# Performance work log

Measured on AMD Instinct MI355X. Metric: run time of the kernel, lower is better.

The kernel has to match this reference:

```python
import jax, jax.numpy as jnp
import numpy as np

N_USER, N_ITEM, D, K, E = 80000, 40000, 128, 10, 2000000

def _mlp(x, w1, b1, w2, b2, w3, b3):
    # MLP from source: linear->tanh->linear->tanh->linear->L2 normalize (eval mode, dropout off)
    x = jnp.tanh(x @ w1 + b1)
    x = jnp.tanh(x @ w2 + b2)
    x = x @ w3 + b3
    return x / jnp.maximum(jnp.linalg.norm(x, axis=-1, keepdims=True), 1e-12)

def setup_inputs() -> dict:
    key = jax.random.key(0)
    ks = jax.random.split(key, 24)
    s = 0.05
    inp = {
        'uemb_s': jax.random.normal(ks[0], (N_USER, D), jnp.float32),
        'iemb_s': jax.random.normal(ks[1], (N_ITEM, D), jnp.float32),
        'uemb_t': jax.random.normal(ks[2], (N_USER, D), jnp.float32),
        'u_emb_sp': jax.random.normal(ks[3], (N_USER, D), jnp.float32),
        'edge_user': jax.random.randint(ks[4], (E,), 0, N_USER, jnp.int32),
        'edge_item': jax.random.randint(ks[5], (E,), 0, N_ITEM, jnp.int32),
        # meta nets
        'Wu': jax.random.normal(ks[6], (4 * D, D), jnp.float32) * s,
        'bu': jnp.zeros((D,), jnp.float32),
        'Wi': jax.random.normal(ks[7], (2 * D, D), jnp.float32) * s,
        'bi': jnp.zeros((D,), jnp.float32),
        # mlp1: D -> D*K -> D//2 -> D*K
        'm1w1': jax.random.normal(ks[8], (D, D * K), jnp.float32) * s,
        'm1b1': jnp.zeros((D * K,), jnp.float32),
        'm1w2': jax.random.normal(ks[9], (D * K, D // 2), jnp.float32) * s,
        'm1b2': jnp.zeros((D // 2,), jnp.float32),
        'm1w3': jax.random.normal(ks[10], (D // 2, D * K), jnp.float32) * s,
        'm1b3': jnp.zeros((D * K,), jnp.float32),
        # mlp2: D -> D*K -> D//2 -> D*K
        'm2w1': jax.random.normal(ks[11], (D, D * K), jnp.float32) * s,
        'm2b1': jnp.zeros((D * K,), jnp.float32),
        'm2w2': jax.random.normal(ks[12], (D * K, D // 2), jnp.float32) * s,
        'm2b2': jnp.zeros((D // 2,), jnp.float32),
        'm2w3': jax.random.normal(ks[13], (D // 2, D * K), jnp.float32) * s,
        'm2b3': jnp.zeros((D * K,), jnp.float32),
    }
    return inp

def reference(uemb_s, iemb_s, uemb_t, u_emb_sp, edge_user, edge_item,
              Wu, bu, Wi, bi,
              m1w1, m1b1, m1w2, m1b2, m1w3, m1b3,
              m2w1, m2b1, m2w2, m2b2, m2w3, m2b3):
    # spmm with all-ones values == gather + segment_sum over the bipartite edge list
    neighbors_u = jax.ops.segment_sum(iemb_s[edge_item], edge_user, num_segments=N_USER)  # [U, D]
    tmp_embu = jax.lax.stop_gradient(
        jnp.concatenate([uemb_s, uemb_t, u_emb_sp, neighbors_u], axis=1)) @ Wu + bu       # [U, D]
    neighbors_i = jax.ops.segment_sum(((uemb_s + u_emb_sp) * 0.5)[edge_user], edge_item,
                                      num_segments=N_ITEM)                               # [I, D]
    tmp_embi = jax.lax.stop_gradient(
        jnp.concatenate([iemb_s, neighbors_i], axis=1)) @ Wi + bi                         # [I, D]
    metau = _mlp(tmp_embu, m1w1, m1b1, m1w2, m1b2, m1w3, m1b3).reshape(-1, D, K)          # [U, D, K]
    metai = _mlp(tmp_embi, m2w1, m2b1, m2w2, m2b2, m2w3, m2b3).reshape(-1, K, D)          # [I, K, D]
    meta_biasu = jnp.mean(metau, axis=0)  # [D, K]
    meta_biasi = jnp.mean(metai, axis=0)  # [K, D]
    low_weightu = jax.nn.softmax(metau + meta_biasu, axis=1)
    low_weighti = jax.nn.softmax(metai + meta_biasi, axis=1)
    return (low_weightu, low_weighti)
```

## Files before the change

kernel.cpp:

```cpp
#include <hip/hip_runtime.h>
#include <hip/hip_bf16.h>

#define D_ 128
#define DK_ 1280
#define K_ 10

typedef __attribute__((ext_vector_type(8))) short bh8;
typedef __attribute__((ext_vector_type(4))) short bh4;
typedef __attribute__((ext_vector_type(4))) float f32x4;

__device__ __forceinline__ short f2b(float f) {
    unsigned u = __builtin_bit_cast(unsigned, f);
    u += 0x7fffu + ((u >> 16) & 1u);
    return (short)(u >> 16);
}
__device__ __forceinline__ float b2f(short s) {
    unsigned u = ((unsigned)(unsigned short)s) << 16;
    return __builtin_bit_cast(float, u);
}
__device__ __forceinline__ float tanh_fast(float x) {
    float e = __expf(2.f * x);
    return 1.f - __fdividef(2.f, e + 1.f);
}
__device__ __forceinline__ f32x4 mfma16(bh8 a, bh8 b, f32x4 c) {
    return __builtin_amdgcn_mfma_f32_16x16x32_bf16(a, b, c, 0, 0, 0);
}

__device__ __forceinline__ int blk_excl_scan(int v, int t) {
    __shared__ int wp[4];
    int lane = t & 63, w = t >> 6;
    int s = v;
    for (int o = 1; o < 64; o <<= 1) {
        int pv = __shfl_up(s, o);
        if (lane >= o) s += pv;
    }
    if (lane == 63) wp[w] = s;
    __syncthreads();
    if (t == 0) {
        int a = 0;
#pragma unroll
        for (int k = 0; k < 4; ++k) { int x = wp[k]; wp[k] = a; a += x; }
    }
    __syncthreads();
    int r = s - v + wp[w];
    __syncthreads();
    return r;
}

__global__ __launch_bounds__(256) void cvt_all(
    const float* __restrict__ us, const float* __restrict__ ut,
    const float* __restrict__ usp, const float* __restrict__ is_,
    short* __restrict__ usb, short* __restrict__ utb,
    short* __restrict__ uspb, short* __restrict__ uavg, short* __restrict__ isb,
    int n4u, int n4i)
{
    int i = blockIdx.x * 256 + threadIdx.x;
    if (i < n4u) {
        float4 a = ((const float4*)us)[i];
        float4 b = ((const float4*)ut)[i];
        float4 c = ((const float4*)usp)[i];
        bh4 sa, sb, sc, sv;
        sa[0] = f2b(a.x); sa[1] = f2b(a.y); sa[2] = f2b(a.z); sa[3] = f2b(a.w);
        sb[0] = f2b(b.x); sb[1] = f2b(b.y); sb[2] = f2b(b.z); sb[3] = f2b(b.w);
        sc[0] = f2b(c.x); sc[1] = f2b(c.y); sc[2] = f2b(c.z); sc[3] = f2b(c.w);
        sv[0] = f2b(0.5f * (a.x + c.x)); sv[1] = f2b(0.5f * (a.y + c.y));
        sv[2] = f2b(0.5f * (a.z + c.z)); sv[3] = f2b(0.5f * (a.w + c.w));
        ((bh4*)usb)[i] = sa; ((bh4*)utb)[i] = sb;
        ((bh4*)uspb)[i] = sc; ((bh4*)uavg)[i] = sv;
    } else if (i < n4u + n4i) {
        int j = i - n4u;
        float4 v = ((const float4*)is_)[j];
        bh4 s;
        s[0] = f2b(v.x); s[1] = f2b(v.y); s[2] = f2b(v.z); s[3] = f2b(v.w);
        ((bh4*)isb)[j] = s;
    }
}

struct PackArgs {
    const float* W[8];
    short* o[8];
    int K[8];
    int N[8];
};
__global__ __launch_bounds__(256) void pack_all(PackArgs pa)
{
    int seg = blockIdx.y;
    int K = pa.K[seg], N = pa.N[seg];
    int total = K * N;
    int o = blockIdx.x * 256 + threadIdx.x;
    if (o >= total) return;
    const float* W = pa.W[seg];
    short* out = pa.o[seg];
    int j    = o & 7;
    int lane = (o >> 3) & 63;
    int rest = o >> 9;
    int KK = K >> 5;
    int kk = rest % KK;
    int tile = rest / KK;
    int k = kk * 32 + (lane >> 4) * 8 + j;
    int n = tile * 16 + (lane & 15);
    out[o] = f2b(W[(size_t)k * N + n]);
}

__global__ __launch_bounds__(256) void bhist_kernel(
    const int* __restrict__ eu, const int* __restrict__ ei,
    int* __restrict__ bcu, int* __restrict__ bci,
    int E, int shu, int shi, int nbu, int nbi)
{
    __shared__ int hu[160], hi[160];
    int t = threadIdx.x;
    int base = blockIdx.x * 4096;
    if (t < 160) { hu[t] = 0; hi[t] = 0; }
    __syncthreads();
    int n = min(4096, E - base);
#pragma unroll 4
    for (int k = 0; k < 16; ++k) {
        int idx = k * 256 + t;
        if (idx < n) {
            atomicAdd(&hu[eu[base + idx] >> shu], 1);
            atomicAdd(&hi[ei[base + idx] >> shi], 1);
        }
    }
    __syncthreads();
    if (t < nbu && hu[t]) atomicAdd(&bcu[t], hu[t]);
    if (t < nbi && hi[t]) atomicAdd(&bci[t], hi[t]);
}

__global__ __launch_bounds__(256) void binit_kernel(
    const int* __restrict__ bcu, int* __restrict__ gcu, int* __restrict__ bbu, int nbu,
    const int* __restrict__ bci, int* __restrict__ gci, int* __restrict__ bbi, int nbi,
    int E)
{
    int t = threadIdx.x;
    {
        int v = (t < nbu) ? bcu[t] : 0;
        int ex = blk_excl_scan(v, t);
        if (t < nbu) { gcu[t] = ex; bbu[t] = ex; }
        if (t == 0) bbu[nbu] = E;
    }
    __syncthreads();
    {
        int v = (t < nbi) ? bci[t] : 0;
        int ex = blk_excl_scan(v, t);
        if (t < nbi) { gci[t] = ex; bbi[t] = ex; }
        if (t == 0) bbi[nbi] = E;
    }
}

__global__ __launch_bounds__(256) void partition_kernel(
    const int* __restrict__ eu, const int* __restrict__ ei,
    int* __restrict__ gcu, int* __restrict__ gci,
    uint2* __restrict__ ebu, uint2* __restrict__ ebi,
    int E, int shu, int shi, int nbu, int nbi)
{
    __shared__ int hu[160], hi[160];
    int t = threadIdx.x;
    int base = blockIdx.x * 4096;
    if (t < 160) { hu[t] = 0; hi[t] = 0; }
    __syncthreads();
    int n = min(4096, E - base);
    int us[16], is_[16];
#pragma unroll 4
    for (int k = 0; k < 16; ++k) {
        int idx = k * 256 + t;
        if (idx < n) {
            us[k] = eu[base + idx];
            is_[k] = ei[base + idx];
            atomicAdd(&hu[us[k] >> shu], 1);
            atomicAdd(&hi[is_[k] >> shi], 1);
        } else us[k] = -1;
    }
    __syncthreads();
    if (t < nbu) { int c = hu[t]; hu[t] = c ? atomicAdd(&gcu[t], c) : 0; }
    if (t < nbi) { int c = hi[t]; hi[t] = c ? atomicAdd(&gci[t], c) : 0; }
    __syncthreads();
#pragma unroll 4
    for (int k = 0; k < 16; ++k) {
        if (us[k] >= 0) {
            int p1 = atomicAdd(&hu[us[k] >> shu], 1);
            ebu[p1] = make_uint2((unsigned)us[k], (unsigned)is_[k]);
            int p2 = atomicAdd(&hi[is_[k] >> shi], 1);
            ebi[p2] = make_uint2((unsigned)is_[k], (unsigned)us[k]);
        }
    }
}

__global__ __launch_bounds__(256) void fill2_all(
    const uint2* __restrict__ ebu, const int* __restrict__ bbu,
    int* __restrict__ off_u, int* __restrict__ end_u, int* __restrict__ adj_u,
    int NBU, int U,
    const uint2* __restrict__ ebi, const int* __restrict__ bbi,
    int* __restrict__ off_i, int* __restrict__ end_i, int* __restrict__ adj_i, int I)
{
    __shared__ int lcnt[512];
    __shared__ int lcur[512];
    bool isU = (int)blockIdx.x < NBU;
    const uint2* ebuf = isU ? ebu : ebi;
    const int* bbase  = isU ? bbu : bbi;
    int* off  = isU ? off_u : off_i;
    int* end_ = isU ? end_u : end_i;
    int* adj  = isU ? adj_u : adj_i;
    int span_sh = isU ? 9 : 8;
    int nrows = isU ? U : I;
    int b = isU ? blockIdx.x : blockIdx.x - NBU;

    int t = threadIdx.x;
    int rbase = b << span_sh;
    int span = min(1 << span_sh, nrows - rbase);
    int regbeg = bbase[b], regend = bbase[b + 1];
    for (int j = t; j < span; j += 256) lcnt[j] = 0;
    __syncthreads();
    for (int e = regbeg + t; e < regend; e += 256)
        atomicAdd(&lcnt[ebuf[e].x - rbase], 1);
    __syncthreads();
    int c0 = (2 * t < span) ? lcnt[2 * t] : 0;
    int c1 = (2 * t + 1 < span) ? lcnt[2 * t + 1] : 0;
    int ex = blk_excl_scan(c0 + c1, t);
    if (2 * t < span) {
        int beg = regbeg + ex;
        off[rbase + 2 * t] = beg;
        end_[rbase + 2 * t] = beg + c0;
        lcur[2 * t] = beg;
    }
    if (2 * t + 1 < span) {
        int beg = regbeg + ex + c0;
        off[rbase + 2 * t + 1] = beg;
        end_[rbase + 2 * t + 1] = beg + c1;
        lcur[2 * t + 1] = beg;
    }
    __syncthreads();
    for (int e = regbeg + t; e < regend; e += 256) {
        uint2 p = ebuf[e];
        int slot = atomicAdd(&lcur[p.x - rbase], 1);
        adj[slot] = (int)p.y;
    }
}

__global__ __launch_bounds__(256) void gather_all(
    const short* __restrict__ embU, const short* __restrict__ embI,
    const int* __restrict__ off_u, const int* __restrict__ end_u, const int* __restrict__ adj_u,
    const int* __restrict__ off_i, const int* __restrict__ end_i, const int* __restrict__ adj_i,
    short* __restrict__ nub, short* __restrict__ nib, int U, int I)
{
    int gw = (blockIdx.x * 256 + threadIdx.x) >> 6;
    int lane = threadIdx.x & 63;
    const short* emb; const int *offp, *endp, *adjp; short* outp; int row;
    if (gw < U)          { emb = embU; offp = off_u; endp = end_u; adjp = adj_u; outp = nub; row = gw; }
    else if (gw < U + I) { emb = embI; offp = off_i; endp = end_i; adjp = adj_i; outp = nib; row = gw - U; }
    else return;

    int beg = offp[row], end = endp[row];
    float ax = 0.f, ay = 0.f;
    int j = beg;
    for (; j + 3 < end; j += 4) {
        unsigned a = *(const unsigned*)(emb + (size_t)adjp[j]     * D_ + lane * 2);
        unsigned b = *(const unsigned*)(emb + (size_t)adjp[j + 1] * D_ + lane * 2);
        unsigned c = *(const unsigned*)(emb + (size_t)adjp[j + 2] * D_ + lane * 2);
        unsigned d = *(const unsigned*)(emb + (size_t)adjp[j + 3] * D_ + lane * 2);
        ax += b2f((short)(a & 0xffff)) + b2f((short)(b & 0xffff))
            + b2f((short)(c & 0xffff)) + b2f((short)(d & 0xffff));
        ay += b2f((short)(a >> 16)) + b2f((short)(b >> 16))
            + b2f((short)(c >> 16)) + b2f((short)(d >> 16));
    }
    for (; j < end; ++j) {
        unsigned a = *(const unsigned*)(emb + (size_t)adjp[j] * D_ + lane * 2);
        ax += b2f((short)(a & 0xffff));
        ay += b2f((short)(a >> 16));
    }
    unsigned o = ((unsigned)(unsigned short)f2b(ay) << 16) | (unsigned short)(unsigned)f2b(ax);
    *(unsigned*)(outp + (size_t)row * D_ + lane * 2) = o;
}

struct MlpArgs {
    const short *uA0, *uA1, *uA2, *uA3;
    const short *iA0, *iA1;
    const short *uWg, *uW1, *uW2, *uW3;
    const short *iWg, *iW1, *iW2, *iW3;
    const float *ubg, *ub1, *ub2, *ub3;
    const float *ibg, *ib1, *ib2, *ib3;
    short *uY, *iY;
    float *uNrm, *iNrm;
    int UB;
};

__global__ __launch_bounds__(256, 4) void fused_mlp_all(MlpArgs P)
{
    __shared__ char pool[35328];
    short* x2   = (short*)pool;
    short* h1q  = (short*)(pool + 8704);
    short* h2   = (short*)(pool + 29696);
    float* wred = (float*)(pool + 34304);

    const int t = threadIdx.x;
    const int l = t & 63;
    const int w = t >> 6;
    const int lr = l & 15;
    const int lg = l >> 4;

    const bool isU = (int)blockIdx.x < P.UB;
    const int bid = isU ? (int)blockIdx.x : (int)blockIdx.x - P.UB;
    const size_t rb0 = (size_t)bid * 32;
    const int KKG  = isU ? 16 : 8;
    const short* Wg = isU ? P.uWg : P.iWg;
    const short* W1 = isU ? P.uW1 : P.iW1;
    const short* W2 = isU ? P.uW2 : P.iW2;
    const short* W3 = isU ? P.uW3 : P.iW3;
    const float* bg = isU ? P.ubg : P.ibg;
    const float* b1 = isU ? P.ub1 : P.ib1;
    const float* b2 = isU ? P.ub2 : P.ib2;
    const float* b3 = isU ? P.ub3 : P.ib3;
    short* Ybf = isU ? P.uY : P.iY;
    float* Nrm = isU ? P.uNrm : P.iNrm;
    const short* srcs[4];
    if (isU) { srcs[0] = P.uA0; srcs[1] = P.uA1; srcs[2] = P.uA2; srcs[3] = P.uA3; }
    else     { srcs[0] = P.iA0; srcs[1] = P.iA1; srcs[2] = P.iA0; srcs[3] = P.iA1; }

    {
        f32x4 acc[2][2] = {{{0,0,0,0},{0,0,0,0}},{{0,0,0,0},{0,0,0,0}}};
        const short* wp = Wg + (size_t)(2 * w) * KKG * 512 + l * 8;
        const short* wq = wp + (size_t)KKG * 512;
        for (int kk = 0; kk < KKG; ++kk) {
            const short* src = srcs[kk >> 2];
            int coff = (kk & 3) * 32 + lg * 8;
            bh8 x0 = *(const bh8*)(src + (rb0 + lr) * D_ + coff);
            bh8 x1 = *(const bh8*)(src + (rb0 + 16 + lr) * D_ + coff);
            bh8 w0 = *(const bh8*)wp; wp += 512;
            bh8 w1 = *(const bh8*)wq; wq += 512;
            acc[0][0] = mfma16(w0, x0, acc[0][0]);
            acc[1][0] = mfma16(w0, x1, acc[1][0]);
            acc[0][1] = mfma16(w1, x0, acc[0][1]);
            acc[1][1] = mfma16(w1, x1, acc[1][1]);
        }
        float4 c0 = *(const float4*)(bg + (2 * w) * 16 + lg * 4);
        float4 c1 = *(const float4*)(bg + (2 * w + 1) * 16 + lg * 4);
#pragma unroll
        for (int rg = 0; rg < 2; ++rg) {
            bh4 p0, p1;
            p0[0] = f2b(acc[rg][0][0] + c0.x); p0[1] = f2b(acc[rg][0][1] + c0.y);
            p0[2] = f2b(acc[rg][0][2] + c0.z); p0[3] = f2b(acc[rg][0][3] + c0.w);
            p1[0] = f2b(acc[rg][1][0] + c1.x); p1[1] = f2b(acc[rg][1][1] + c1.y);
            p1[2] = f2b(acc[rg][1][2] + c1.z); p1[3] = f2b(acc[rg][1][3] + c1.w);
            *(bh4*)(x2 + (rg * 16 + lr) * 136 + (2 * w) * 16 + lg * 4) = p0;
            *(bh4*)(x2 + (rg * 16 + lr) * 136 + (2 * w + 1) * 16 + lg * 4) = p1;
        }
    }
    __syncthreads();

    bh8 xf[2][4];
#pragma unroll
    for (int rg = 0; rg < 2; ++rg)
#pragma unroll
        for (int kk = 0; kk < 4; ++kk)
            xf[rg][kk] = *(const bh8*)(x2 + (rg * 16 + lr) * 136 + kk * 32 + lg * 8);

    f32x4 c2[2][2] = {{{0,0,0,0},{0,0,0,0}},{{0,0,0,0},{0,0,0,0}}};
#pragma unroll 1
    for (int q = 0; q < 4; ++q) {
        const short* wp = W1 + (size_t)(q * 20 + w * 5) * 2048 + l * 8;
        const float* bp = b1 + (q * 20 + w * 5) * 16 + lg * 4;
#pragma unroll 1
        for (int tt = 0; tt < 5; ++tt) {
            f32x4 a0 = {0,0,0,0}, a1 = a0;
#pragma unroll
            for (int kk = 0; kk < 4; ++kk) {
                bh8 wf = *(const bh8*)wp; wp += 512;
                a0 = mfma16(wf, xf[0][kk], a0);
                a1 = mfma16(wf, xf[1][kk], a1);
            }
            float4 bv = *(const float4*)bp; bp += 16;
            bh4 pk0, pk1;
            pk0[0] = f2b(tanh_fast(a0[0] + bv.x)); pk0[1] = f2b(tanh_fast(a0[1] + bv.y));
            pk0[2] = f2b(tanh_fast(a0[2] + bv.z)); pk0[3] = f2b(tanh_fast(a0[3] + bv.w));
            pk1[0] = f2b(tanh_fast(a1[0] + bv.x)); pk1[1] = f2b(tanh_fast(a1[1] + bv.y));
            pk1[2] = f2b(tanh_fast(a1[2] + bv.z)); pk1[3] = f2b(tanh_fast(a1[3] + bv.w));
            int lt = w * 5 + tt;
            *(bh4*)(h1q + lr * 328 + lt * 16 + lg * 4) = pk0;
            *(bh4*)(h1q + (16 + lr) * 328 + lt * 16 + lg * 4) = pk1;
        }
        __syncthreads();
        const short* wp2 = W2 + (size_t)(w * 40 + q * 10) * 512 + l * 8;
        const short* hq0 = h1q + lr * 328 + lg * 8;
        const short* hq1 = h1q + (16 + lr) * 328 + lg * 8;
#pragma unroll 2
        for (int kk = 0; kk < 10; ++kk) {
            bh8 wf = *(const bh8*)wp2; wp2 += 512;
            bh8 h0 = *(const bh8*)(hq0 + kk * 32);
            bh8 h1v = *(const bh8*)(hq1 + kk * 32);
            if (kk & 1) { c2[0][1] = mfma16(wf, h0, c2[0][1]); c2[1][1] = mfma16(wf, h1v, c2[1][1]); }
            else        { c2[0][0] = mfma16(wf, h0, c2[0][0]); c2[1][0] = mfma16(wf, h1v, c2[1][0]); }
        }
        __syncthreads();
    }

    {
        float4 bv = *(const float4*)(b2 + w * 16 + lg * 4);
#pragma unroll
        for (int rg = 0; rg < 2; ++rg) {
            bh4 p2;
            p2[0] = f2b(tanh_fast(c2[rg][0][0] + c2[rg][1][0] + bv.x));
            p2[1] = f2b(tanh_fast(c2[rg][0][1] + c2[rg][1][1] + bv.y));
            p2[2] = f2b(tanh_fast(c2[rg][0][2] + c2[rg][1][2] + bv.z));
            p2[3] = f2b(tanh_fast(c2[rg][0][3] + c2[rg][1][3] + bv.w));
            *(bh4*)(h2 + (rg * 16 + lr) * 72 + w * 16 + lg * 4) = p2;
        }
    }
    __syncthreads();

    {
        bh8 hf[2][2];
#pragma unroll
        for (int rg = 0; rg < 2; ++rg) {
            hf[rg][0] = *(const bh8*)(h2 + (rg * 16 + lr) * 72 + lg * 8);
            hf[rg][1] = *(const bh8*)(h2 + (rg * 16 + lr) * 72 + 32 + lg * 8);
        }
        float ssq0 = 0.f, ssq1 = 0.f;
        const short* wp3 = W3 + (size_t)(w * 20) * 1024 + l * 8;
        const float* bp3 = b3 + w * 320 + lg * 4;
        short* dst0 = Ybf + (rb0 + lr) * DK_ + w * 320 + lg * 4;
        short* dst1 = Ybf + (rb0 + 16 + lr) * DK_ + w * 320 + lg * 4;
#pragma unroll 2
        for (int tt = 0; tt < 20; ++tt) {
            bh8 w0 = *(const bh8*)(wp3 + tt * 1024);
            bh8 w1 = *(const bh8*)(wp3 + tt * 1024 + 512);
            float4 bv = *(const float4*)(bp3 + tt * 16);
            f32x4 a0 = {0,0,0,0}, a1 = a0;
            a0 = mfma16(w0, hf[0][0], a0); a0 = mfma16(w1, hf[0][1], a0);
            a1 = mfma16(w0, hf[1][0], a1); a1 = mfma16(w1, hf[1][1], a1);
            float v00 = a0[0] + bv.x, v01 = a0[1] + bv.y, v02 = a0[2] + bv.z, v03 = a0[3] + bv.w;
            float v10 = a1[0] + bv.x, v11 = a1[1] + bv.y, v12 = a1[2] + bv.z, v13 = a1[3] + bv.w;
            ssq0 = fmaf(v00, v00, ssq0); ssq0 = fmaf(v01, v01, ssq0);
            ssq0 = fmaf(v02, v02, ssq0); ssq0 = fmaf(v03, v03, ssq0);
            ssq1 = fmaf(v10, v10, ssq1); ssq1 = fmaf(v11, v11, ssq1);
            ssq1 = fmaf(v12, v12, ssq1); ssq1 = fmaf(v13, v13, ssq1);
            bh4 o0, o1;
            o0[0] = f2b(v00); o0[1] = f2b(v01); o0[2] = f2b(v02); o0[3] = f2b(v03);
            o1[0] = f2b(v10); o1[1] = f2b(v11); o1[2] = f2b(v12); o1[3] = f2b(v13);
            *(bh4*)(dst0 + tt * 16) = o0;
            *(bh4*)(dst1 + tt * 16) = o1;
        }
        ssq0 += __shfl_xor(ssq0, 16); ssq0 += __shfl_xor(ssq0, 32);
        ssq1 += __shfl_xor(ssq1, 16); ssq1 += __shfl_xor(ssq1, 32);
        if (l < 16) {
            wred[w * 32 + l] = ssq0;
            wred[w * 32 + 16 + l] = ssq1;
        }
    }
    __syncthreads();
    if (t < 32) {
        float s = wred[t] + wred[32 + t] + wred[64 + t] + wred[96 + t];
        Nrm[rb0 + t] = 1.f / fmaxf(sqrtf(s), 1e-12f);
    }
}

__global__ __launch_bounds__(256) void finalize_bias(
    const short* __restrict__ Yu, const short* __restrict__ Yi,
    const float* __restrict__ nrmU, const float* __restrict__ nrmI,
    float* __restrict__ bsu, float* __restrict__ bsi, int U, int I, int NCH)
{
    int z = blockIdx.y;
    const short* Y = z ? Yi : Yu;
    const float* nr = z ? nrmI : nrmU;
    float* dst = z ? bsi : bsu;
    int M = z ? I : U;
    int chunk = (M + NCH - 1) / NCH;
    int r0 = blockIdx.x * chunk;
    int r1 = min(M, r0 + chunk);
    if (r0 >= r1) return;
    int t = threadIdx.x;
    float s0 = 0.f, s1 = 0.f, s2 = 0.f, s3 = 0.f, s4 = 0.f;
    for (int r = r0; r < r1; ++r) {
        const short* row = Y + (size_t)r * DK_;
        float nv = nr[r];
        s0 += b2f(row[t]) * nv;
        s1 += b2f(row[256 + t]) * nv;
        s2 += b2f(row[512 + t]) * nv;
        s3 += b2f(row[768 + t]) * nv;
        s4 += b2f(row[1024 + t]) * nv;
    }
    atomicAdd(&dst[t], s0);
    atomicAdd(&dst[256 + t], s1);
    atomicAdd(&dst[512 + t], s2);
    atomicAdd(&dst[768 + t], s3);
    atomicAdd(&dst[1024 + t], s4);
}

__global__ __launch_bounds__(64) void softmax_all(
    const short* __restrict__ Yu, const short* __restrict__ Yi,
    const float* __restrict__ nrmU, const float* __restrict__ nrmI,
    const float* __restrict__ bsu, const float* __restrict__ bsi,
    float invU, float invI,
    float* __restrict__ outu, float* __restrict__ outi, int U, int I)
{
    __shared__ float rowb[DK_];
    int b = blockIdx.x;
    int t = threadIdx.x;
    if (b < U) {
        size_t base = (size_t)b * DK_;
        float nrm = nrmU[b];
        for (int i = t; i < DK_ / 4; i += 64) {
            uint2 a = ((const uint2*)(Yu + base))[i];
            float4 bv = ((const float4*)bsu)[i];
            rowb[4 * i + 0] = b2f((short)(a.x & 0xffff)) * nrm + bv.x * invU;
            rowb[4 * i + 1] = b2f((short)(a.x >> 16))    * nrm + bv.y * invU;
            rowb[4 * i + 2] = b2f((short)(a.y & 0xffff)) * nrm + bv.z * invU;
            rowb[4 * i + 3] = b2f((short)(a.y >> 16))    * nrm + bv.w * invU;
        }
        __syncthreads();
#pragma unroll 1
        for (int k = 0; k < K_; ++k) {
            float v0 = rowb[t * K_ + k];
            float v1 = rowb[(t + 64) * K_ + k];
            float m = fmaxf(v0, v1);
            for (int off = 32; off; off >>= 1) m = fmaxf(m, __shfl_xor(m, off));
            float e0 = expf(v0 - m), e1 = expf(v1 - m);
            float s = e0 + e1;
            for (int off = 32; off; off >>= 1) s += __shfl_xor(s, off);
            float rs = 1.f / s;
            rowb[t * K_ + k] = e0 * rs;
            rowb[(t + 64) * K_ + k] = e1 * rs;
        }
        __syncthreads();
        for (int i = t; i < DK_ / 4; i += 64)
            ((float4*)(outu + base))[i] = ((const float4*)rowb)[i];
    } else {
        int it = b - U;
        if (it >= I) return;
        size_t base = (size_t)it * DK_;
        float nrm = nrmI[it];
        float v0[K_], v1[K_];
        float m0 = -1e30f, m1 = -1e30f;
#pragma unroll
        for (int k = 0; k < K_; ++k) {
            unsigned a = *(const unsigned*)(Yi + base + k * D_ + 2 * t);
            float2 bv = ((const float2*)(bsi + k * D_))[t];
            v0[k] = b2f((short)(a & 0xffff)) * nrm + bv.x * invI;
            v1[k] = b2f((short)(a >> 16))    * nrm + bv.y * invI;
            m0 = fmaxf(m0, v0[k]); m1 = fmaxf(m1, v1[k]);
        }
        float s0 = 0.f, s1 = 0.f;
#pragma unroll
        for (int k = 0; k < K_; ++k) {
            v0[k] = expf(v0[k] - m0); s0 += v0[k];
            v1[k] = expf(v1[k] - m1); s1 += v1[k];
        }
        float r0 = 1.f / s0, r1 = 1.f / s1;
#pragma unroll
        for (int k = 0; k < K_; ++k) {
            float2 o; o.x = v0[k] * r0; o.y = v1[k] * r1;
            ((float2*)(outi + base + k * D_))[t] = o;
        }
    }
}

extern "C" void kernel_launch(void* const* d_in, const int* in_sizes, int n_in,
                              void* d_out, int out_size, void* d_ws, size_t ws_size,
                              hipStream_t stream)
{
    const float* uemb_s   = (const float*)d_in[0];
    const float* iemb_s   = (const float*)d_in[1];
    const float* uemb_t   = (const float*)d_in[2];
    const float* u_emb_sp = (const float*)d_in[3];
    const int*   eu       = (const int*)d_in[4];
    const int*   ei       = (const int*)d_in[5];
    const float* Wu  = (const float*)d_in[6];
    const float* bu  = (const float*)d_in[7];
    const float* Wi  = (const float*)d_in[8];
    const float* bi  = (const float*)d_in[9];
    const float* m1w1 = (const float*)d_in[10];
    const float* m1b1 = (const float*)d_in[11];
    const float* m1w2 = (const float*)d_in[12];
    const float* m1b2 = (const float*)d_in[13];
    const float* m1w3 = (const float*)d_in[14];
    const float* m1b3 = (const float*)d_in[15];
    const float* m2w1 = (const float*)d_in[16];
    const float* m2b1 = (const float*)d_in[17];
    const float* m2w2 = (const float*)d_in[18];
    const float* m2b2 = (const float*)d_in[19];
    const float* m2w3 = (const float*)d_in[20];
    const float* m2b3 = (const float*)d_in[21];

    const int U = in_sizes[0] / D_;
    const int I = in_sizes[1] / D_;
    const int E = in_sizes[4];

    const int SHU = 9, SHI = 8;
    const int NBU = (U + 511) >> 9;
    const int NBI = (I + 255) >> 8;
    const int UB = U / 32, IB = I / 32;

    char* p = (char*)d_ws;
    auto alloc = [&](size_t bytes) { char* r = p; p += (bytes + 255) & ~(size_t)255; return r; };

    short* usb  = (short*)alloc((size_t)U * D_ * 2);
    short* utb  = (short*)alloc((size_t)U * D_ * 2);
    short* uspb = (short*)alloc((size_t)U * D_ * 2);
    short* uavg = (short*)alloc((size_t)U * D_ * 2);
    short* isb  = (short*)alloc((size_t)I * D_ * 2);
    short* nub  = (short*)alloc((size_t)U * D_ * 2);
    short* nib  = (short*)alloc((size_t)I * D_ * 2);
    short* ybu  = (short*)alloc((size_t)U * DK_ * 2);
    short* ybi  = (short*)alloc((size_t)I * DK_ * 2);
    float* nrmU = (float*)alloc((size_t)U * 4);
    float* nrmI = (float*)alloc((size_t)I * 4);
    short* WgU  = (short*)alloc(512 * 128 * 2);
    short* WgI  = (short*)alloc(256 * 128 * 2);
    short* W1U  = (short*)alloc(128 * 1280 * 2);
    short* W2U  = (short*)alloc(1280 * 64 * 2);
    short* W3U  = (short*)alloc(64 * 1280 * 2);
    short* W1I  = (short*)alloc(128 * 1280 * 2);
    short* W2I  = (short*)alloc(1280 * 64 * 2);
    short* W3I  = (short*)alloc(64 * 1280 * 2);
    int*   zbuf = (int*)alloc((320 + 2 * DK_) * 4);
    int* bcnt_u = zbuf;
    int* bcnt_i = zbuf + 160;
    float* bsu  = (float*)(zbuf + 320);
    float* bsi  = bsu + DK_;
    int* gcur_u = (int*)alloc(160 * 4);
    int* gcur_i = (int*)alloc(160 * 4);
    int* bbase_u = (int*)alloc(161 * 4);
    int* bbase_i = (int*)alloc(161 * 4);
    int* off_u  = (int*)alloc((size_t)U * 4);
    int* end_u  = (int*)alloc((size_t)U * 4);
    int* off_i  = (int*)alloc((size_t)I * 4);
    int* end_i  = (int*)alloc((size_t)I * 4);
    uint2* ebu  = (uint2*)alloc((size_t)E * 8);
    uint2* ebi  = (uint2*)alloc((size_t)E * 8);
    int* adj_u  = (int*)alloc((size_t)E * 4);
    int* adj_i  = (int*)alloc((size_t)E * 4);

    float* outu = (float*)d_out;
    float* outi = outu + (size_t)U * DK_;

    hipMemsetAsync(zbuf, 0, (320 + 2 * DK_) * 4, stream);

    int n4u = U * D_ / 4, n4i = I * D_ / 4;
    cvt_all<<<(n4u + n4i + 255) / 256, 256, 0, stream>>>(
        uemb_s, uemb_t, u_emb_sp, iemb_s, usb, utb, uspb, uavg, isb, n4u, n4i);

    PackArgs pa;
    pa.W[0] = Wu;   pa.o[0] = WgU; pa.K[0] = 512;  pa.N[0] = 128;
    pa.W[1] = Wi;   pa.o[1] = WgI; pa.K[1] = 256;  pa.N[1] = 128;
    pa.W[2] = m1w1; pa.o[2] = W1U; pa.K[2] = 128;  pa.N[2] = 1280;
    pa.W[3] = m1w2; pa.o[3] = W2U; pa.K[3] = 1280; pa.N[3] = 64;
    pa.W[4] = m1w3; pa.o[4] = W3U; pa.K[4] = 64;   pa.N[4] = 1280;
    pa.W[5] = m2w1; pa.o[5] = W1I; pa.K[5] = 128;  pa.N[5] = 1280;
    pa.W[6] = m2w2; pa.o[6] = W2I; pa.K[6] = 1280; pa.N[6] = 64;
    pa.W[7] = m2w3; pa.o[7] = W3I; pa.K[7] = 64;   pa.N[7] = 1280;
    pack_all<<<dim3(640, 8), 256, 0, stream>>>(pa);

    int pb = (E + 4095) / 4096;
    bhist_kernel<<<pb, 256, 0, stream>>>(eu, ei, bcnt_u, bcnt_i, E, SHU, SHI, NBU, NBI);
    binit_kernel<<<1, 256, 0, stream>>>(bcnt_u, gcur_u, bbase_u, NBU,
                                        bcnt_i, gcur_i, bbase_i, NBI, E);
    partition_kernel<<<pb, 256, 0, stream>>>(eu, ei, gcur_u, gcur_i, ebu, ebi,
                                             E, SHU, SHI, NBU, NBI);
    fill2_all<<<NBU + NBI, 256, 0, stream>>>(ebu, bbase_u, off_u, end_u, adj_u, NBU, U,
                                             ebi, bbase_i, off_i, end_i, adj_i, I);

    gather_all<<<(U + I + 3) / 4, 256, 0, stream>>>(
        isb, uavg, off_u, end_u, adj_u, off_i, end_i, adj_i, nub, nib, U, I);

    MlpArgs ma;
    ma.uA0 = usb; ma.uA1 = utb; ma.uA2 = uspb; ma.uA3 = nub;
    ma.iA0 = isb; ma.iA1 = nib;
    ma.uWg = WgU; ma.uW1 = W1U; ma.uW2 = W2U; ma.uW3 = W3U;
    ma.iWg = WgI; ma.iW1 = W1I; ma.iW2 = W2I; ma.iW3 = W3I;
    ma.ubg = bu; ma.ub1 = m1b1; ma.ub2 = m1b2; ma.ub3 = m1b3;
    ma.ibg = bi; ma.ib1 = m2b1; ma.ib2 = m2b2; ma.ib3 = m2b3;
    ma.uY = ybu; ma.iY = ybi;
    ma.uNrm = nrmU; ma.iNrm = nrmI;
    ma.UB = UB;
    fused_mlp_all<<<UB + IB, 256, 0, stream>>>(ma);

    finalize_bias<<<dim3(256, 2), 256, 0, stream>>>(ybu, ybi, nrmU, nrmI, bsu, bsi, U, I, 256);

    softmax_all<<<U + I, 64, 0, stream>>>(ybu, ybi, nrmU, nrmI, bsu, bsi,
                                          1.0f / (float)U, 1.0f / (float)I, outu, outi, U, I);
}
```

Baseline: 929.4 us.

## Pack edge buckets into 32-bit words and give each wave its own MLP rows

Partition buckets now store each edge as one 32-bit word: the local row offset sits in the high bits and the neighbour index in the low bits. This halves bucket write and read traffic in the partition and fill kernels. The fused MLP is restructured so each wave handles 16 independent rows (64 rows per block) and computes every output tile itself, which removes all block-level __syncthreads and the cross-wave reduction. The trade-off is that each wave reloads the full weight matrices for only 16 rows, which raises weight traffic per row and the register pressure from 8 accumulators.

```diff
diff --git a/kernel.cpp b/kernel.cpp
--- a/kernel.cpp
+++ b/kernel.cpp
@@ -150,7 +150,7 @@
 __global__ __launch_bounds__(256) void partition_kernel(
     const int* __restrict__ eu, const int* __restrict__ ei,
     int* __restrict__ gcu, int* __restrict__ gci,
-    uint2* __restrict__ ebu, uint2* __restrict__ ebi,
+    unsigned* __restrict__ ebu, unsigned* __restrict__ ebi,
     int E, int shu, int shi, int nbu, int nbi)
 {
     __shared__ int hu[160], hi[160];
@@ -178,29 +178,31 @@
     for (int k = 0; k < 16; ++k) {
         if (us[k] >= 0) {
             int p1 = atomicAdd(&hu[us[k] >> shu], 1);
-            ebu[p1] = make_uint2((unsigned)us[k], (unsigned)is_[k]);
+            ebu[p1] = ((unsigned)(us[k] & 511) << 16) | (unsigned)is_[k];
             int p2 = atomicAdd(&hi[is_[k] >> shi], 1);
-            ebi[p2] = make_uint2((unsigned)is_[k], (unsigned)us[k]);
+            ebi[p2] = ((unsigned)(is_[k] & 255) << 17) | (unsigned)us[k];
         }
     }
 }
 
 __global__ __launch_bounds__(256) void fill2_all(
-    const uint2* __restrict__ ebu, const int* __restrict__ bbu,
+    const unsigned* __restrict__ ebu, const int* __restrict__ bbu,
     int* __restrict__ off_u, int* __restrict__ end_u, int* __restrict__ adj_u,
     int NBU, int U,
-    const uint2* __restrict__ ebi, const int* __restrict__ bbi,
+    const unsigned* __restrict__ ebi, const int* __restrict__ bbi,
     int* __restrict__ off_i, int* __restrict__ end_i, int* __restrict__ adj_i, int I)
 {
     __shared__ int lcnt[512];
     __shared__ int lcur[512];
     bool isU = (int)blockIdx.x < NBU;
-    const uint2* ebuf = isU ? ebu : ebi;
+    const unsigned* ebuf = isU ? ebu : ebi;
     const int* bbase  = isU ? bbu : bbi;
     int* off  = isU ? off_u : off_i;
     int* end_ = isU ? end_u : end_i;
     int* adj  = isU ? adj_u : adj_i;
     int span_sh = isU ? 9 : 8;
+    int pay_sh = isU ? 16 : 17;
+    unsigned pmask = (1u << pay_sh) - 1u;
     int nrows = isU ? U : I;
     int b = isU ? blockIdx.x : blockIdx.x - NBU;
 
@@ -211,7 +213,7 @@
     for (int j = t; j < span; j += 256) lcnt[j] = 0;
     __syncthreads();
     for (int e = regbeg + t; e < regend; e += 256)
-        atomicAdd(&lcnt[ebuf[e].x - rbase], 1);
+        atomicAdd(&lcnt[ebuf[e] >> pay_sh], 1);
     __syncthreads();
     int c0 = (2 * t < span) ? lcnt[2 * t] : 0;
     int c1 = (2 * t + 1 < span) ? lcnt[2 * t + 1] : 0;
@@ -230,9 +232,9 @@
     }
     __syncthreads();
     for (int e = regbeg + t; e < regend; e += 256) {
-        uint2 p = ebuf[e];
-        int slot = atomicAdd(&lcur[p.x - rbase], 1);
-        adj[slot] = (int)p.y;
+        unsigned p = ebuf[e];
+        int slot = atomicAdd(&lcur[p >> pay_sh], 1);
+        adj[slot] = (int)(p & pmask);
     }
 }
 
@@ -285,21 +287,20 @@
 
 __global__ __launch_bounds__(256, 4) void fused_mlp_all(MlpArgs P)
 {
-    __shared__ char pool[35328];
-    short* x2   = (short*)pool;
-    short* h1q  = (short*)(pool + 8704);
-    short* h2   = (short*)(pool + 29696);
-    float* wred = (float*)(pool + 34304);
+    __shared__ short h1c_s[4][16 * 136];
+    __shared__ short h2_s[4][16 * 72];
 
     const int t = threadIdx.x;
     const int l = t & 63;
     const int w = t >> 6;
     const int lr = l & 15;
     const int lg = l >> 4;
+    short* h1c = h1c_s[w];
+    short* h2w = h2_s[w];
 
     const bool isU = (int)blockIdx.x < P.UB;
     const int bid = isU ? (int)blockIdx.x : (int)blockIdx.x - P.UB;
-    const size_t rb0 = (size_t)bid * 32;
+    const size_t rb0 = (size_t)bid * 64 + w * 16;
     const int KKG  = isU ? 16 : 8;
     const short* Wg = isU ? P.uWg : P.iWg;
     const short* W1 = isU ? P.uW1 : P.iW1;
@@ -316,139 +317,93 @@
     else     { srcs[0] = P.iA0; srcs[1] = P.iA1; srcs[2] = P.iA0; srcs[3] = P.iA1; }
 
     {
-        f32x4 acc[2][2] = {{{0,0,0,0},{0,0,0,0}},{{0,0,0,0},{0,0,0,0}}};
-        const short* wp = Wg + (size_t)(2 * w) * KKG * 512 + l * 8;
-        const short* wq = wp + (size_t)KKG * 512;
+        f32x4 acc[8] = {{0,0,0,0},{0,0,0,0},{0,0,0,0},{0,0,0,0},
+                        {0,0,0,0},{0,0,0,0},{0,0,0,0},{0,0,0,0}};
         for (int kk = 0; kk < KKG; ++kk) {
-            const short* src = srcs[kk >> 2];
-            int coff = (kk & 3) * 32 + lg * 8;
-            bh8 x0 = *(const bh8*)(src + (rb0 + lr) * D_ + coff);
-            bh8 x1 = *(const bh8*)(src + (rb0 + 16 + lr) * D_ + coff);
-            bh8 w0 = *(const bh8*)wp; wp += 512;
-            bh8 w1 = *(const bh8*)wq; wq += 512;
-            acc[0][0] = mfma16(w0, x0, acc[0][0]);
-            acc[1][0] = mfma16(w0, x1, acc[1][0]);
-            acc[0][1] = mfma16(w1, x0, acc[0][1]);
-            acc[1][1] = mfma16(w1, x1, acc[1][1]);
-        }
-        float4 c0 = *(const float4*)(bg + (2 * w) * 16 + lg * 4);
-        float4 c1 = *(const float4*)(bg + (2 * w + 1) * 16 + lg * 4);
-#pragma unroll
-        for (int rg = 0; rg < 2; ++rg) {
-            bh4 p0, p1;
-            p0[0] = f2b(acc[rg][0][0] + c0.x); p0[1] = f2b(acc[rg][0][1] + c0.y);
-            p0[2] = f2b(acc[rg][0][2] + c0.z); p0[3] = f2b(acc[rg][0][3] + c0.w);
-            p1[0] = f2b(acc[rg][1][0] + c1.x); p1[1] = f2b(acc[rg][1][1] + c1.y);
-            p1[2] = f2b(acc[rg][1][2] + c1.z); p1[3] = f2b(acc[rg][1][3] + c1.w);
-            *(bh4*)(x2 + (rg * 16 + lr) * 136 + (2 * w) * 16 + lg * 4) = p0;
-            *(bh4*)(x2 + (rg * 16 + lr) * 136 + (2 * w + 1) * 16 + lg * 4) = p1;
-        }
-    }
-    __syncthreads();
-
-    bh8 xf[2][4];
-#pragma unroll
-    for (int rg = 0; rg < 2; ++rg)
-#pragma unroll
-        for (int kk = 0; kk < 4; ++kk)
-            xf[rg][kk] = *(const bh8*)(x2 + (rg * 16 + lr) * 136 + kk * 32 + lg * 8);
-
-    f32x4 c2[2][2] = {{{0,0,0,0},{0,0,0,0}},{{0,0,0,0},{0,0,0,0}}};
+            bh8 xv = *(const bh8*)(srcs[kk >> 2] + (rb0 + lr) * D_ + (kk & 3) * 32 + lg * 8);
+            const short* wp = Wg + (size_t)kk * 512 + (size_t)l * 8;
+#pragma unroll
+            for (int tile = 0; tile < 8; ++tile)
+                acc[tile] = mfma16(*(const bh8*)(wp + (size_t)tile * KKG * 512), xv, acc[tile]);
+        }
+#pragma unroll
+        for (int tile = 0; tile < 8; ++tile) {
+            float4 bv = *(const float4*)(bg + tile * 16 + lg * 4);
+            bh4 pk;
+            pk[0] = f2b(acc[tile][0] + bv.x); pk[1] = f2b(acc[tile][1] + bv.y);
+            pk[2] = f2b(acc[tile][2] + bv.z); pk[3] = f2b(acc[tile][3] + bv.w);
+            *(bh4*)(h1c + lr * 136 + tile * 16 + lg * 4) = pk;
+        }
+    }
+
+    bh8 xf[4];
+#pragma unroll
+    for (int kk = 0; kk < 4; ++kk)
+        xf[kk] = *(const bh8*)(h1c + lr * 136 + kk * 32 + lg * 8);
+
+    f32x4 c2[4] = {{0,0,0,0},{0,0,0,0},{0,0,0,0},{0,0,0,0}};
 #pragma unroll 1
-    for (int q = 0; q < 4; ++q) {
-        const short* wp = W1 + (size_t)(q * 20 + w * 5) * 2048 + l * 8;
-        const float* bp = b1 + (q * 20 + w * 5) * 16 + lg * 4;
-#pragma unroll 1
-        for (int tt = 0; tt < 5; ++tt) {
-            f32x4 a0 = {0,0,0,0}, a1 = a0;
-#pragma unroll
-            for (int kk = 0; kk < 4; ++kk) {
-                bh8 wf = *(const bh8*)wp; wp += 512;
-                a0 = mfma16(wf, xf[0][kk], a0);
-                a1 = mfma16(wf, xf[1][kk], a1);
-            }
-            float4 bv = *(const float4*)bp; bp += 16;
-            bh4 pk0, pk1;
-            pk0[0] = f2b(tanh_fast(a0[0] + bv.x)); pk0[1] = f2b(tanh_fast(a0[1] + bv.y));
-            pk0[2] = f2b(tanh_fast(a0[2] + bv.z)); pk0[3] = f2b(tanh_fast(a0[3] + bv.w));
-            pk1[0] = f2b(tanh_fast(a1[0] + bv.x)); pk1[1] = f2b(tanh_fast(a1[1] + bv.y));
-            pk1[2] = f2b(tanh_fast(a1[2] + bv.z)); pk1[3] = f2b(tanh_fast(a1[3] + bv.w));
-            int lt = w * 5 + tt;
-            *(bh4*)(h1q + lr * 328 + lt * 16 + lg * 4) = pk0;
-            *(bh4*)(h1q + (16 + lr) * 328 + lt * 16 + lg * 4) = pk1;
-        }
-        __syncthreads();
-        const short* wp2 = W2 + (size_t)(w * 40 + q * 10) * 512 + l * 8;
-        const short* hq0 = h1q + lr * 328 + lg * 8;
-        const short* hq1 = h1q + (16 + lr) * 328 + lg * 8;
-#pragma unroll 2
-        for (int kk = 0; kk < 10; ++kk) {
-            bh8 wf = *(const bh8*)wp2; wp2 += 512;
-            bh8 h0 = *(const bh8*)(hq0 + kk * 32);
-            bh8 h1v = *(const bh8*)(hq1 + kk * 32);
-            if (kk & 1) { c2[0][1] = mfma16(wf, h0, c2[0][1]); c2[1][1] = mfma16(wf, h1v, c2[1][1]); }
-            else        { c2[0][0] = mfma16(wf, h0, c2[0][0]); c2[1][0] = mfma16(wf, h1v, c2[1][0]); }
-        }
-        __syncthreads();
+    for (int q = 0; q < 10; ++q) {
+#pragma unroll
+        for (int tile = 0; tile < 8; ++tile) {
+            int gt = q * 8 + tile;
+            const short* wp = W1 + (size_t)gt * 2048 + l * 8;
+            f32x4 a = {0, 0, 0, 0};
+#pragma unroll
+            for (int kk = 0; kk < 4; ++kk)
+                a = mfma16(*(const bh8*)(wp + kk * 512), xf[kk], a);
+            float4 bv = *(const float4*)(b1 + gt * 16 + lg * 4);
+            bh4 pk;
+            pk[0] = f2b(tanh_fast(a[0] + bv.x));
+            pk[1] = f2b(tanh_fast(a[1] + bv.y));
+            pk[2] = f2b(tanh_fast(a[2] + bv.z));
+            pk[3] = f2b(tanh_fast(a[3] + bv.w));
+            *(bh4*)(h1c + lr * 136 + tile * 16 + lg * 4) = pk;
+        }
+#pragma unroll
+        for (int kk = 0; kk < 4; ++kk) {
+            bh8 hf = *(const bh8*)(h1c + lr * 136 + kk * 32 + lg * 8);
+            const short* wp2 = W2 + (size_t)(q * 4 + kk) * 512 + l * 8;
+#pragma unroll
+            for (int ht = 0; ht < 4; ++ht)
+                c2[ht] = mfma16(*(const bh8*)(wp2 + (size_t)ht * 40 * 512), hf, c2[ht]);
+        }
+    }
+
+#pragma unroll
+    for (int ht = 0; ht < 4; ++ht) {
+        float4 bv = *(const float4*)(b2 + ht * 16 + lg * 4);
+        bh4 p2;
+        p2[0] = f2b(tanh_fast(c2[ht][0] + bv.x));
+        p2[1] = f2b(tanh_fast(c2[ht][1] + bv.y));
+        p2[2] = f2b(tanh_fast(c2[ht][2] + bv.z));
+        p2[3] = f2b(tanh_fast(c2[ht][3] + bv.w));
+        *(bh4*)(h2w + lr * 72 + ht * 16 + lg * 4) = p2;
     }
 
     {
-        float4 bv = *(const float4*)(b2 + w * 16 + lg * 4);
-#pragma unroll
-        for (int rg = 0; rg < 2; ++rg) {
-            bh4 p2;
-            p2[0] = f2b(tanh_fast(c2[rg][0][0] + c2[rg][1][0] + bv.x));
-            p2[1] = f2b(tanh_fast(c2[rg][0][1] + c2[rg][1][1] + bv.y));
-            p2[2] = f2b(tanh_fast(c2[rg][0][2] + c2[rg][1][2] + bv.z));
-            p2[3] = f2b(tanh_fast(c2[rg][0][3] + c2[rg][1][3] + bv.w));
-            *(bh4*)(h2 + (rg * 16 + lr) * 72 + w * 16 + lg * 4) = p2;
-        }
-    }
-    __syncthreads();
-
-    {
-        bh8 hf[2][2];
-#pragma unroll
-        for (int rg = 0; rg < 2; ++rg) {
-            hf[rg][0] = *(const bh8*)(h2 + (rg * 16 + lr) * 72 + lg * 8);
-            hf[rg][1] = *(const bh8*)(h2 + (rg * 16 + lr) * 72 + 32 + lg * 8);
-        }
-        float ssq0 = 0.f, ssq1 = 0.f;
-        const short* wp3 = W3 + (size_t)(w * 20) * 1024 + l * 8;
-        const float* bp3 = b3 + w * 320 + lg * 4;
-        short* dst0 = Ybf + (rb0 + lr) * DK_ + w * 320 + lg * 4;
-        short* dst1 = Ybf + (rb0 + 16 + lr) * DK_ + w * 320 + lg * 4;
-#pragma unroll 2
-        for (int tt = 0; tt < 20; ++tt) {
-            bh8 w0 = *(const bh8*)(wp3 + tt * 1024);
-            bh8 w1 = *(const bh8*)(wp3 + tt * 1024 + 512);
-            float4 bv = *(const float4*)(bp3 + tt * 16);
-            f32x4 a0 = {0,0,0,0}, a1 = a0;
-            a0 = mfma16(w0, hf[0][0], a0); a0 = mfma16(w1, hf[0][1], a0);
-            a1 = mfma16(w0, hf[1][0], a1); a1 = mfma16(w1, hf[1][1], a1);
-            float v00 = a0[0] + bv.x, v01 = a0[1] + bv.y, v02 = a0[2] + bv.z, v03 = a0[3] + bv.w;
-            float v10 = a1[0] + bv.x, v11 = a1[1] + bv.y, v12 = a1[2] + bv.z, v13 = a1[3] + bv.w;
-            ssq0 = fmaf(v00, v00, ssq0); ssq0 = fmaf(v01, v01, ssq0);
-            ssq0 = fmaf(v02, v02, ssq0); ssq0 = fmaf(v03, v03, ssq0);
-            ssq1 = fmaf(v10, v10, ssq1); ssq1 = fmaf(v11, v11, ssq1);
-            ssq1 = fmaf(v12, v12, ssq1); ssq1 = fmaf(v13, v13, ssq1);
-            bh4 o0, o1;
-            o0[0] = f2b(v00); o0[1] = f2b(v01); o0[2] = f2b(v02); o0[3] = f2b(v03);
-            o1[0] = f2b(v10); o1[1] = f2b(v11); o1[2] = f2b(v12); o1[3] = f2b(v13);
-            *(bh4*)(dst0 + tt * 16) = o0;
-            *(bh4*)(dst1 + tt * 16) = o1;
-        }
-        ssq0 += __shfl_xor(ssq0, 16); ssq0 += __shfl_xor(ssq0, 32);
-        ssq1 += __shfl_xor(ssq1, 16); ssq1 += __shfl_xor(ssq1, 32);
-        if (l < 16) {
-            wred[w * 32 + l] = ssq0;
-            wred[w * 32 + 16 + l] = ssq1;
-        }
-    }
-    __syncthreads();
-    if (t < 32) {
-        float s = wred[t] + wred[32 + t] + wred[64 + t] + wred[96 + t];
-        Nrm[rb0 + t] = 1.f / fmaxf(sqrtf(s), 1e-12f);
+        bh8 hf0 = *(const bh8*)(h2w + lr * 72 + lg * 8);
+        bh8 hf1 = *(const bh8*)(h2w + lr * 72 + 32 + lg * 8);
+        float ssq = 0.f;
+        short* dst = Ybf + (rb0 + lr) * DK_ + lg * 4;
+#pragma unroll 4
+        for (int tt = 0; tt < 80; ++tt) {
+            const short* wp3 = W3 + (size_t)tt * 1024 + l * 8;
+            f32x4 a = {0, 0, 0, 0};
+            a = mfma16(*(const bh8*)wp3, hf0, a);
+            a = mfma16(*(const bh8*)(wp3 + 512), hf1, a);
+            float4 bv = *(const float4*)(b3 + tt * 16 + lg * 4);
+            float v0 = a[0] + bv.x, v1 = a[1] + bv.y;
+            float v2 = a[2] + bv.z, v3 = a[3] + bv.w;
+            ssq = fmaf(v0, v0, ssq); ssq = fmaf(v1, v1, ssq);
+            ssq = fmaf(v2, v2, ssq); ssq = fmaf(v3, v3, ssq);
+            bh4 o;
+            o[0] = f2b(v0); o[1] = f2b(v1); o[2] = f2b(v2); o[3] = f2b(v3);
+            *(bh4*)(dst + tt * 16) = o;
+        }
+        ssq += __shfl_xor(ssq, 16);
+        ssq += __shfl_xor(ssq, 32);
+        if (l < 16) Nrm[rb0 + l] = 1.f / fmaxf(sqrtf(ssq), 1e-12f);
     }
 }
 
@@ -586,7 +541,7 @@
     const int SHU = 9, SHI = 8;
     const int NBU = (U + 511) >> 9;
     const int NBI = (I + 255) >> 8;
-    const int UB = U / 32, IB = I / 32;
+    const int UB = U / 64, IB = I / 64;
 
     char* p = (char*)d_ws;
     auto alloc = [&](size_t bytes) { char* r = p; p += (bytes + 255) & ~(size_t)255; return r; };
@@ -623,8 +578,8 @@
     int* end_u  = (int*)alloc((size_t)U * 4);
     int* off_i  = (int*)alloc((size_t)I * 4);
     int* end_i  = (int*)alloc((size_t)I * 4);
-    uint2* ebu  = (uint2*)alloc((size_t)E * 8);
-    uint2* ebi  = (uint2*)alloc((size_t)E * 8);
+    unsigned* ebu = (unsigned*)alloc((size_t)E * 4);
+    unsigned* ebi = (unsigned*)alloc((size_t)E * 4);
     int* adj_u  = (int*)alloc((size_t)E * 4);
     int* adj_i  = (int*)alloc((size_t)E * 4);
 
```

After: 1.078 ms. 1.16x slower.
